# Optimization experiments

Measured on AMD Instinct MI355X. Metric: run time of the kernel, lower is better.

Reference implementation:

```python
import jax, jax.numpy as jnp
import numpy as np

H = 16  # headNum
D = 1024  # d_model
DK = D // H


def setup_inputs() -> dict:
    key = jax.random.key(0)
    ks = jax.random.split(key, 11)
    B, S = 2, 2048
    scale = 1.0 / np.sqrt(D)
    inp = {
        'query': jax.random.normal(ks[0], (B, S, D), jnp.float32),
        'key':   jax.random.normal(ks[1], (B, S, D), jnp.float32),
        'value': jax.random.normal(ks[2], (B, S, D), jnp.float32),
        # nn.Linear params: W is [out, in], y = x @ W.T + b
        'Wq': jax.random.normal(ks[3], (D, D), jnp.float32) * scale,
        'bq': jnp.zeros((D,), jnp.float32),
        'Wk': jax.random.normal(ks[4], (D, D), jnp.float32) * scale,
        'bk': jnp.zeros((D,), jnp.float32),
        'Wv': jax.random.normal(ks[5], (D, D), jnp.float32) * scale,
        'bv': jnp.zeros((D,), jnp.float32),
        'Wo': jax.random.normal(ks[6], (D, D), jnp.float32) * scale,
        'bo': jnp.zeros((D,), jnp.float32),
    }
    return inp


def reference(query, key, value, Wq, bq, Wk, bk, Wv, bv, Wo, bo):
    B, S, _ = query.shape
    # projections (torch Linear: x @ W.T + b), split heads -> [B, H, S, DK]
    q = (query @ Wq.T + bq).reshape(B, S, H, DK).transpose(0, 2, 1, 3)
    k = (key   @ Wk.T + bk).reshape(B, S, H, DK).transpose(0, 2, 1, 3)
    v = (value @ Wv.T + bv).reshape(B, S, H, DK).transpose(0, 2, 1, 3)
    # scores [B, H, S, S] = Q K^T / sqrt(d_k)  (fully materialized, as in source)
    scores = jnp.einsum('bhqd,bhkd->bhqk', q, k) * (DK ** -0.5)
    p_attn = jax.nn.softmax(scores, axis=-1)  # dropout = identity (eval)
    x = jnp.einsum('bhqk,bhkd->bhqd', p_attn, v)
    x = x.transpose(0, 2, 1, 3).reshape(B, S, H * DK)
    return x @ Wo.T + bo
```

## Files before the change

kernel.cpp:

```cpp
#include <hip/hip_runtime.h>

#define BATCH 2
#define SEQ   2048
#define NH    16
#define DK    64
#define DM    1024
#define MROWS 4096
#define NX    4194304
#define NW    1048576


typedef __attribute__((ext_vector_type(8))) short bf16x8;
typedef __attribute__((ext_vector_type(4))) short bf16x4;
typedef __attribute__((ext_vector_type(4))) float f32x4;
typedef __attribute__((ext_vector_type(4))) unsigned short us16x4;

#if __has_builtin(__builtin_amdgcn_mfma_f32_16x16x16bf16_1k)
#define MFMA16(a, b, c) __builtin_amdgcn_mfma_f32_16x16x16bf16_1k(a, b, c, 0, 0, 0)
#else
#define MFMA16(a, b, c) (c)
#endif

__device__ __forceinline__ unsigned short f2bf(float f) {
  unsigned int u = __builtin_bit_cast(unsigned int, f);
  u += 0x7FFFu + ((u >> 16) & 1u);
  return (unsigned short)(u >> 16);
}

__device__ __forceinline__ void g2l16(void* lds, const void* g) {
  __builtin_amdgcn_global_load_lds(
      (const __attribute__((address_space(1))) void*)g,
      (__attribute__((address_space(3))) void*)lds, 16, 0, 0);
}

__global__ __launch_bounds__(256) void cast_all(
    const float* __restrict__ q, const float* __restrict__ k, const float* __restrict__ v,
    const float* __restrict__ wq, const float* __restrict__ wk,
    const float* __restrict__ wv, const float* __restrict__ wo,
    unsigned short* __restrict__ dst) {
  size_t e = ((size_t)blockIdx.x * 256 + threadIdx.x) * 4;
  const float* src;
  if      (e < (size_t)NX)        src = q  + e;
  else if (e < (size_t)2*NX)      src = k  + (e - (size_t)NX);
  else if (e < (size_t)3*NX)      src = v  + (e - (size_t)2*NX);
  else if (e < (size_t)3*NX+NW)   src = wq + (e - (size_t)3*NX);
  else if (e < (size_t)3*NX+2*NW) src = wk + (e - (size_t)3*NX-NW);
  else if (e < (size_t)3*NX+3*NW) src = wv + (e - (size_t)3*NX-2*NW);
  else                            src = wo + (e - (size_t)3*NX-3*NW);
  float4 f = *(const float4*)src;
  us16x4 o;
  o[0] = f2bf(f.x); o[1] = f2bf(f.y); o[2] = f2bf(f.z); o[3] = f2bf(f.w);
  *(us16x4*)(dst + e) = o;
}

template <int MODE>
__global__ __launch_bounds__(256) void gemm_bt(
    const unsigned short* __restrict__ Xbase, const unsigned short* __restrict__ Wbase,
    const float* __restrict__ b0, const float* __restrict__ b1, const float* __restrict__ b2,
    unsigned short* __restrict__ qkv_dst, float* __restrict__ fout, float qscale) {
  const int tid  = threadIdx.x;
  const int lane = tid & 63;
  const int w    = tid >> 6;
  const int wm   = w >> 1, wn = w & 1;
  const int x15  = lane & 15, quad = lane >> 4;
  const int row0 = blockIdx.x * 128;
  const int col0 = blockIdx.y * 128;
  const int z    = blockIdx.z;

  const unsigned short* A  = Xbase + (size_t)z * NX;
  const unsigned short* Wp = Wbase + (size_t)z * NW;
  const float* bias = (MODE == 0) ? (z == 0 ? b0 : (z == 1 ? b1 : b2)) : b0;
  const float zs = (MODE == 0 && z == 0) ? qscale : 1.0f;

  __shared__ __align__(16) unsigned short At[128 * 32];
  __shared__ __align__(16) unsigned short Bt[128 * 32];

  f32x4 acc[4][4] = {};

  for (int kt = 0; kt < DM; kt += 32) {
#pragma unroll
    for (int j = 0; j < 2; ++j) {
      int e = (j * 256 + tid) * 8;
      int r = e >> 5, c = e & 31;
      g2l16(&At[e], A  + (size_t)(row0 + r) * DM + kt + c);
      g2l16(&Bt[e], Wp + (size_t)(col0 + r) * DM + kt + c);
    }
    __syncthreads();
    bf16x8 af[4], bf[4];
#pragma unroll
    for (int i = 0; i < 4; ++i) {
      af[i] = *(const bf16x8*)&At[(wm * 64 + i * 16 + x15) * 32 + quad * 8];
      bf[i] = *(const bf16x8*)&Bt[(wn * 64 + i * 16 + x15) * 32 + quad * 8];
    }
#pragma unroll
    for (int i = 0; i < 4; ++i)
#pragma unroll
      for (int jn = 0; jn < 4; ++jn)
        acc[i][jn] = __builtin_amdgcn_mfma_f32_16x16x32_bf16(af[i], bf[jn], acc[i][jn], 0, 0, 0);
    __syncthreads();
  }

#pragma unroll
  for (int jn = 0; jn < 4; ++jn) {
    const int n = col0 + wn * 64 + jn * 16 + x15;
    const float bv = bias[n];
#pragma unroll
    for (int i = 0; i < 4; ++i) {
      const int m0 = row0 + wm * 64 + i * 16 + quad * 4;
      if (MODE == 0 && z == 2) {
        us16x4 pk;
#pragma unroll
        for (int r = 0; r < 4; ++r) pk[r] = f2bf(acc[i][jn][r] + bv);
        const int b = m0 >> 11, s = m0 & 2047;
        const int h = n >> 6,  dk = n & 63;
        *(us16x4*)&qkv_dst[(size_t)2 * NX + (((size_t)(b * NH + h) * DK + dk) << 11) + s] = pk;
      } else {
#pragma unroll
        for (int r = 0; r < 4; ++r) {
          const int m = m0 + r;
          float val = (acc[i][jn][r] + bv) * zs;
          if (MODE == 0) {
            const int b = m >> 11, s = m & 2047;
            const int h = n >> 6,  dk = n & 63;
            qkv_dst[(size_t)z * NX + (((size_t)(b * NH + h) * SEQ + s) << 6) + dk] = f2bf(val);
          } else {
            fout[(size_t)m * DM + n] = val;
          }
        }
      }
    }
  }
}

__global__ __launch_bounds__(256) void attn(
    const unsigned short* __restrict__ Qb, const unsigned short* __restrict__ Kb,
    const unsigned short* __restrict__ VTb, unsigned short* __restrict__ AO) {
  const int tid  = threadIdx.x;
  const int lane = tid & 63;
  const int w    = tid >> 6;
  const int x15  = lane & 15, quad = lane >> 4;
  const int qt = blockIdx.x;
  const int h  = blockIdx.y;
  const int b  = blockIdx.z;
  const size_t bh = ((size_t)(b * NH + h)) * SEQ * DK;
  const unsigned short* Q  = Qb  + bh;
  const unsigned short* K  = Kb  + bh;
  const unsigned short* VT = VTb + bh;
  const int q0 = qt * 128 + w * 32;

  __shared__ __align__(16) unsigned short Kl[64 * 64];
  __shared__ __align__(16) unsigned short Vl[64 * 64];

  bf16x8 qf[2][2];
#pragma unroll
  for (int mi = 0; mi < 2; ++mi)
#pragma unroll
    for (int ks = 0; ks < 2; ++ks)
      qf[mi][ks] = *(const bf16x8*)&Q[(size_t)(q0 + mi * 16 + x15) * DK + ks * 32 + quad * 8];

  f32x4 po[2][4] = {};
  float lp[2] = {0.0f, 0.0f};

  const int sK0 = tid >> 3,          sK1 = (tid + 256) >> 3;
  const int dgK0 = (tid & 7) ^ (sK0 & 7), dgK1 = (tid & 7) ^ (sK1 & 7);
  const int dV0 = sK0, dV1 = sK1;
  const int sgV0 = dgK0, sgV1 = dgK1;

  for (int s0 = 0; s0 < SEQ; s0 += 64) {
    __syncthreads();
    g2l16(&Kl[(size_t)tid * 8],         K + (size_t)(s0 + sK0) * DK + dgK0 * 8);
    g2l16(&Kl[(size_t)(tid + 256) * 8], K + (size_t)(s0 + sK1) * DK + dgK1 * 8);
    g2l16(&Vl[(size_t)tid * 8],         VT + (size_t)dV0 * SEQ + s0 + sgV0 * 8);
    g2l16(&Vl[(size_t)(tid + 256) * 8], VT + (size_t)dV1 * SEQ + s0 + sgV1 * 8);
    __syncthreads();

#pragma unroll
    for (int sh = 0; sh < 4; ++sh) {
      const int srow = sh * 16 + x15;
      const int kbase = srow * 8;
      bf16x8 kf0 = *(const bf16x8*)&Kl[(kbase + ((0 + quad) ^ (x15 & 7))) * 8];
      bf16x8 kf1 = *(const bf16x8*)&Kl[(kbase + ((4 + quad) ^ (x15 & 7))) * 8];

      bf16x4 pf[2];
#pragma unroll
      for (int mi = 0; mi < 2; ++mi) {
        f32x4 sacc = {};
        sacc = __builtin_amdgcn_mfma_f32_16x16x32_bf16(kf0, qf[mi][0], sacc, 0, 0, 0);
        sacc = __builtin_amdgcn_mfma_f32_16x16x32_bf16(kf1, qf[mi][1], sacc, 0, 0, 0);
        bf16x4 pk;
#pragma unroll
        for (int r = 0; r < 4; ++r) {
          float p = __builtin_amdgcn_exp2f(sacc[r]);
          lp[mi] += p;
          pk[r] = (short)f2bf(p);
        }
        pf[mi] = pk;
      }

#pragma unroll
      for (int nt = 0; nt < 4; ++nt) {
        const int d = nt * 16 + x15;
        const int sg = (sh * 2 + (quad >> 1)) ^ (d & 7);
        bf16x4 vf = *(const bf16x4*)&Vl[(d * 8 + sg) * 8 + (quad & 1) * 4];
        po[0][nt] = MFMA16(vf, pf[0], po[0][nt]);
        po[1][nt] = MFMA16(vf, pf[1], po[1][nt]);
      }
    }
  }

#pragma unroll
  for (int mi = 0; mi < 2; ++mi) {
    lp[mi] += __shfl_xor(lp[mi], 16);
    lp[mi] += __shfl_xor(lp[mi], 32);
  }

#pragma unroll
  for (int mi = 0; mi < 2; ++mi) {
    const float inv = 1.0f / lp[mi];
    const int s = q0 + mi * 16 + x15;
#pragma unroll
    for (int nt = 0; nt < 4; ++nt) {
      us16x4 pk;
#pragma unroll
      for (int r = 0; r < 4; ++r) pk[r] = f2bf(po[mi][nt][r] * inv);
      const int d = nt * 16 + quad * 4;
      *(us16x4*)&AO[((size_t)(b * SEQ + s)) * DM + h * DK + d] = pk;
    }
  }
}

extern "C" void kernel_launch(void* const* d_in, const int* in_sizes, int n_in,
                              void* d_out, int out_size, void* d_ws, size_t ws_size,
                              hipStream_t stream) {
  const float* q  = (const float*)d_in[0];
  const float* k  = (const float*)d_in[1];
  const float* v  = (const float*)d_in[2];
  const float* wq = (const float*)d_in[3];
  const float* bq = (const float*)d_in[4];
  const float* wk = (const float*)d_in[5];
  const float* bk = (const float*)d_in[6];
  const float* wv = (const float*)d_in[7];
  const float* bv = (const float*)d_in[8];
  const float* wo = (const float*)d_in[9];
  const float* bo = (const float*)d_in[10];
  float* out = (float*)d_out;

  unsigned short* ws = (unsigned short*)d_ws;
  unsigned short* Xq = ws;
  unsigned short* Wb = ws + (size_t)3 * NX;
  unsigned short* Qb = ws + (size_t)3 * NX + 4 * NW;
  unsigned short* AO = Qb + (size_t)3 * NX;

  const float qscale = 0.125f * 1.4426950408889634f;

  cast_all<<<16384, 256, 0, stream>>>(q, k, v, wq, wk, wv, wo, ws);
  gemm_bt<0><<<dim3(32, 8, 3), 256, 0, stream>>>(Xq, Wb, bq, bk, bv, Qb, nullptr, qscale);
  attn<<<dim3(16, 16, 2), 256, 0, stream>>>(Qb, Qb + (size_t)NX, Qb + (size_t)2 * NX, AO);
  gemm_bt<1><<<dim3(32, 8, 1), 256, 0, stream>>>(AO, Wb + (size_t)3 * NW, bo, bo, bo,
                                                 nullptr, out, 1.0f);
}
```

Baseline: 250.3 us.

## Double-buffer LDS in GEMM and attention, compute softmax denominator via MFMA

Both the projection GEMM and the attention kernel now use two LDS buffers. The next tile's global-to-LDS loads are issued before computing on the current tile, and each loop iteration uses one barrier instead of two. In attention, the exp values are packed to bf16 by truncation through a byte permute rather than round-to-nearest. The row sum is computed with an extra MFMA against a ones vector instead of scalar adds and cross-lane shuffles, so the denominator is taken from the same bf16-rounded probabilities used for P·V. The cost is doubled LDS use, which may lower occupancy, and slightly different rounding.

```diff
diff --git a/kernel.cpp b/kernel.cpp
--- a/kernel.cpp
+++ b/kernel.cpp
@@ -9,11 +9,11 @@
 #define NX    4194304
 #define NW    1048576
 
-
 typedef __attribute__((ext_vector_type(8))) short bf16x8;
 typedef __attribute__((ext_vector_type(4))) short bf16x4;
 typedef __attribute__((ext_vector_type(4))) float f32x4;
 typedef __attribute__((ext_vector_type(4))) unsigned short us16x4;
+typedef __attribute__((ext_vector_type(2))) unsigned int u32x2;
 
 #if __has_builtin(__builtin_amdgcn_mfma_f32_16x16x16bf16_1k)
 #define MFMA16(a, b, c) __builtin_amdgcn_mfma_f32_16x16x16bf16_1k(a, b, c, 0, 0, 0)
@@ -25,6 +25,16 @@
   unsigned int u = __builtin_bit_cast(unsigned int, f);
   u += 0x7FFFu + ((u >> 16) & 1u);
   return (unsigned short)(u >> 16);
+}
+
+__device__ __forceinline__ unsigned int pkbf(float hi, float lo) {
+#if __has_builtin(__builtin_amdgcn_perm)
+  return __builtin_amdgcn_perm(__builtin_bit_cast(unsigned int, hi),
+                               __builtin_bit_cast(unsigned int, lo), 0x07060302u);
+#else
+  return (__builtin_bit_cast(unsigned int, hi) & 0xffff0000u) |
+         (__builtin_bit_cast(unsigned int, lo) >> 16);
+#endif
 }
 
 __device__ __forceinline__ void g2l16(void* lds, const void* g) {
@@ -72,32 +82,37 @@
   const float* bias = (MODE == 0) ? (z == 0 ? b0 : (z == 1 ? b1 : b2)) : b0;
   const float zs = (MODE == 0 && z == 0) ? qscale : 1.0f;
 
-  __shared__ __align__(16) unsigned short At[128 * 32];
-  __shared__ __align__(16) unsigned short Bt[128 * 32];
+  __shared__ __align__(16) unsigned short At[2][128 * 32];
+  __shared__ __align__(16) unsigned short Bt[2][128 * 32];
 
   f32x4 acc[4][4] = {};
 
-  for (int kt = 0; kt < DM; kt += 32) {
+  auto stage = [&](int buf, int kt) {
 #pragma unroll
     for (int j = 0; j < 2; ++j) {
       int e = (j * 256 + tid) * 8;
       int r = e >> 5, c = e & 31;
-      g2l16(&At[e], A  + (size_t)(row0 + r) * DM + kt + c);
-      g2l16(&Bt[e], Wp + (size_t)(col0 + r) * DM + kt + c);
-    }
+      g2l16(&At[buf][e], A  + (size_t)(row0 + r) * DM + kt + c);
+      g2l16(&Bt[buf][e], Wp + (size_t)(col0 + r) * DM + kt + c);
+    }
+  };
+
+  stage(0, 0);
+  for (int it = 0; it < DM / 32; ++it) {
+    const int cur = it & 1;
     __syncthreads();
-    bf16x8 af[4], bf[4];
+    if (it + 1 < DM / 32) stage(cur ^ 1, (it + 1) * 32);
+    bf16x8 af[4], bfv[4];
 #pragma unroll
     for (int i = 0; i < 4; ++i) {
-      af[i] = *(const bf16x8*)&At[(wm * 64 + i * 16 + x15) * 32 + quad * 8];
-      bf[i] = *(const bf16x8*)&Bt[(wn * 64 + i * 16 + x15) * 32 + quad * 8];
+      af[i]  = *(const bf16x8*)&At[cur][(wm * 64 + i * 16 + x15) * 32 + quad * 8];
+      bfv[i] = *(const bf16x8*)&Bt[cur][(wn * 64 + i * 16 + x15) * 32 + quad * 8];
     }
 #pragma unroll
     for (int i = 0; i < 4; ++i)
 #pragma unroll
       for (int jn = 0; jn < 4; ++jn)
-        acc[i][jn] = __builtin_amdgcn_mfma_f32_16x16x32_bf16(af[i], bf[jn], acc[i][jn], 0, 0, 0);
-    __syncthreads();
+        acc[i][jn] = __builtin_amdgcn_mfma_f32_16x16x32_bf16(af[i], bfv[jn], acc[i][jn], 0, 0, 0);
   }
 
 #pragma unroll
@@ -148,8 +163,8 @@
   const unsigned short* VT = VTb + bh;
   const int q0 = qt * 128 + w * 32;
 
-  __shared__ __align__(16) unsigned short Kl[64 * 64];
-  __shared__ __align__(16) unsigned short Vl[64 * 64];
+  __shared__ __align__(16) unsigned short Kl[2][64 * 64];
+  __shared__ __align__(16) unsigned short Vl[2][64 * 64];
 
   bf16x8 qf[2][2];
 #pragma unroll
@@ -159,27 +174,30 @@
       qf[mi][ks] = *(const bf16x8*)&Q[(size_t)(q0 + mi * 16 + x15) * DK + ks * 32 + quad * 8];
 
   f32x4 po[2][4] = {};
-  float lp[2] = {0.0f, 0.0f};
+  f32x4 pol[2] = {};
+  const bf16x4 vone = {(short)0x3F80, (short)0x3F80, (short)0x3F80, (short)0x3F80};
 
   const int sK0 = tid >> 3,          sK1 = (tid + 256) >> 3;
   const int dgK0 = (tid & 7) ^ (sK0 & 7), dgK1 = (tid & 7) ^ (sK1 & 7);
-  const int dV0 = sK0, dV1 = sK1;
-  const int sgV0 = dgK0, sgV1 = dgK1;
-
+
+  auto stageKV = [&](int buf, int s0) {
+    g2l16(&Kl[buf][(size_t)tid * 8],         K + (size_t)(s0 + sK0) * DK + dgK0 * 8);
+    g2l16(&Kl[buf][(size_t)(tid + 256) * 8], K + (size_t)(s0 + sK1) * DK + dgK1 * 8);
+    g2l16(&Vl[buf][(size_t)tid * 8],         VT + (size_t)sK0 * SEQ + s0 + dgK0 * 8);
+    g2l16(&Vl[buf][(size_t)(tid + 256) * 8], VT + (size_t)sK1 * SEQ + s0 + dgK1 * 8);
+  };
+
+  stageKV(0, 0);
   for (int s0 = 0; s0 < SEQ; s0 += 64) {
+    const int cur = (s0 >> 6) & 1;
     __syncthreads();
-    g2l16(&Kl[(size_t)tid * 8],         K + (size_t)(s0 + sK0) * DK + dgK0 * 8);
-    g2l16(&Kl[(size_t)(tid + 256) * 8], K + (size_t)(s0 + sK1) * DK + dgK1 * 8);
-    g2l16(&Vl[(size_t)tid * 8],         VT + (size_t)dV0 * SEQ + s0 + sgV0 * 8);
-    g2l16(&Vl[(size_t)(tid + 256) * 8], VT + (size_t)dV1 * SEQ + s0 + sgV1 * 8);
-    __syncthreads();
+    if (s0 + 64 < SEQ) stageKV(cur ^ 1, s0 + 64);
 
 #pragma unroll
     for (int sh = 0; sh < 4; ++sh) {
-      const int srow = sh * 16 + x15;
-      const int kbase = srow * 8;
-      bf16x8 kf0 = *(const bf16x8*)&Kl[(kbase + ((0 + quad) ^ (x15 & 7))) * 8];
-      bf16x8 kf1 = *(const bf16x8*)&Kl[(kbase + ((4 + quad) ^ (x15 & 7))) * 8];
+      const int kbase = (sh * 16 + x15) * 8;
+      bf16x8 kf0 = *(const bf16x8*)&Kl[cur][(kbase + ((0 + quad) ^ (x15 & 7))) * 8];
+      bf16x8 kf1 = *(const bf16x8*)&Kl[cur][(kbase + ((4 + quad) ^ (x15 & 7))) * 8];
 
       bf16x4 pf[2];
 #pragma unroll
@@ -187,21 +205,22 @@
         f32x4 sacc = {};
         sacc = __builtin_amdgcn_mfma_f32_16x16x32_bf16(kf0, qf[mi][0], sacc, 0, 0, 0);
         sacc = __builtin_amdgcn_mfma_f32_16x16x32_bf16(kf1, qf[mi][1], sacc, 0, 0, 0);
-        bf16x4 pk;
-#pragma unroll
-        for (int r = 0; r < 4; ++r) {
-          float p = __builtin_amdgcn_exp2f(sacc[r]);
-          lp[mi] += p;
-          pk[r] = (short)f2bf(p);
-        }
-        pf[mi] = pk;
+        float p0 = __builtin_amdgcn_exp2f(sacc[0]);
+        float p1 = __builtin_amdgcn_exp2f(sacc[1]);
+        float p2 = __builtin_amdgcn_exp2f(sacc[2]);
+        float p3 = __builtin_amdgcn_exp2f(sacc[3]);
+        u32x2 uu;
+        uu[0] = pkbf(p1, p0);
+        uu[1] = pkbf(p3, p2);
+        pf[mi] = __builtin_bit_cast(bf16x4, uu);
+        pol[mi] = MFMA16(vone, pf[mi], pol[mi]);
       }
 
 #pragma unroll
       for (int nt = 0; nt < 4; ++nt) {
         const int d = nt * 16 + x15;
         const int sg = (sh * 2 + (quad >> 1)) ^ (d & 7);
-        bf16x4 vf = *(const bf16x4*)&Vl[(d * 8 + sg) * 8 + (quad & 1) * 4];
+        bf16x4 vf = *(const bf16x4*)&Vl[cur][(d * 8 + sg) * 8 + (quad & 1) * 4];
         po[0][nt] = MFMA16(vf, pf[0], po[0][nt]);
         po[1][nt] = MFMA16(vf, pf[1], po[1][nt]);
       }
@@ -210,13 +229,7 @@
 
 #pragma unroll
   for (int mi = 0; mi < 2; ++mi) {
-    lp[mi] += __shfl_xor(lp[mi], 16);
-    lp[mi] += __shfl_xor(lp[mi], 32);
-  }
-
-#pragma unroll
-  for (int mi = 0; mi < 2; ++mi) {
-    const float inv = 1.0f / lp[mi];
+    const float inv = 1.0f / pol[mi][0];
     const int s = q0 + mi * 16 + x15;
 #pragma unroll
     for (int nt = 0; nt < 4; ++nt) {
```

New measurement: 238.0 us. 4.9% less time.
